# Kernel optimization log

Hardware: AMD Instinct MI355X
Metric: run time of the kernel (lower is better)

Reference implementation:

```python
import jax, jax.numpy as jnp
import numpy as np
from jax import lax

BS = 256
EPS = 1e-5  # torch LayerNorm default


def _layernorm(x, g, b):
    m = jnp.mean(x, axis=-1, keepdims=True)
    v = jnp.var(x, axis=-1, keepdims=True)
    return (x - m) / jnp.sqrt(v + EPS) * g + b


def _conv(x, w, b):
    y = lax.conv_general_dilated(x, w, (1, 1), 'VALID',
                                 dimension_numbers=('NCHW', 'OIHW', 'NCHW'))
    return y + b[None, :, None, None]


def _maxpool2(x):
    return lax.reduce_window(x, -jnp.inf, lax.max, (1, 1, 2, 2), (1, 1, 2, 2), 'VALID')


def setup_inputs() -> dict:
    key = jax.random.key(0)
    ks = iter(jax.random.split(key, 64))
    def rn(shape, scale=0.05):
        return jax.random.normal(next(ks), shape, dtype=jnp.float32) * scale
    return dict(
        t=jax.random.uniform(next(ks), (BS, 128, 128), dtype=jnp.float32) * 255.0,
        conv1_w=rn((32, 1, 3, 3)), conv1_b=rn((32,)),
        conv2_w=rn((32, 32, 3, 3)), conv2_b=rn((32,)),
        exp_w=rn((36, 64)), exp_b=rn((64,)),
        # 16 tile-attention modules x 4 heads x (64 -> 16)
        mh_wq=rn((16, 4, 64, 16)), mh_bq=rn((16, 4, 16)),
        mh_wk=rn((16, 4, 64, 16)), mh_bk=rn((16, 4, 16)),
        mh_wv=rn((16, 4, 64, 16)), mh_bv=rn((16, 4, 16)),
        mh_wo=rn((16, 64, 64)), mh_bo=rn((16, 64)),
        ln1_g=jnp.ones((64,), jnp.float32), ln1_b=jnp.zeros((64,), jnp.float32),
        # 2 XL layers x 8 heads x (2048 -> 256)
        xl_wq=rn((2, 8, 2048, 256)), xl_bq=rn((2, 8, 256)),
        xl_wk=rn((2, 8, 2048, 256)), xl_bk=rn((2, 8, 256)),
        xl_wv=rn((2, 8, 2048, 256)), xl_bv=rn((2, 8, 256)),
        xl_wo=rn((2, 2048, 2048)), xl_bo=rn((2, 2048)),
        xln_g=jnp.ones((2, 2048), jnp.float32), xln_b=jnp.zeros((2, 2048), jnp.float32),
        fl1_w=rn((32768, 512)), fl1_b=rn((512,)),
        fl2_w=rn((512, 128)), fl2_b=rn((128,)),
        fl3_w=rn((128, 25)), fl3_b=rn((25,)),
    )


def reference(t, conv1_w, conv1_b, conv2_w, conv2_b, exp_w, exp_b,
              mh_wq, mh_bq, mh_wk, mh_bk, mh_wv, mh_bv, mh_wo, mh_bo,
              ln1_g, ln1_b,
              xl_wq, xl_bq, xl_wk, xl_bk, xl_wv, xl_bv, xl_wo, xl_bo,
              xln_g, xln_b, fl1_w, fl1_b, fl2_w, fl2_b, fl3_w, fl3_b):
    # Eval-mode forward with discard_mem=True (fresh KV memory): every
    # AttentionHead attends over the current step only; dropout = identity.
    bs = t.shape[0]
    x = t / 255.0
    # 4x4 tiling of 32x32 patches -> (bs*16, 1, 32, 32)
    sliced = x.reshape(bs, 4, 32, 4, 32).transpose(0, 1, 3, 2, 4)
    x = sliced.reshape(bs * 16, 1, 32, 32)
    u = _maxpool2(_conv(x, conv1_w, conv1_b))        # (bs*16, 32, 15, 15)
    u = _maxpool2(_conv(u, conv2_w, conv2_b))        # (bs*16, 32, 6, 6)
    u = u.reshape(bs * 16, 32, 36)
    u = jax.nn.relu(u @ exp_w + exp_b)               # (bs*16, 32, 64)
    u = u.reshape(16, bs, 32, 64)                    # raw reshape, as in source

    # 16 multihead modules, 4 heads each, d_feature=16, seq_len=32
    q = jnp.einsum('mbsd,mhdf->mbhsf', u, mh_wq) + mh_bq[:, None, :, None, :]
    k = jnp.einsum('mbsd,mhdf->mbhsf', u, mh_wk) + mh_bk[:, None, :, None, :]
    v = jnp.einsum('mbsd,mhdf->mbhsf', u, mh_wv) + mh_bv[:, None, :, None, :]
    a = jax.nn.softmax(jnp.einsum('mbhsf,mbhtf->mbhst', q, k) / jnp.sqrt(16.0), axis=-1)
    o = jnp.einsum('mbhst,mbhtf->mbhsf', a, v)
    o = o.transpose(0, 1, 3, 2, 4).reshape(16, bs, 32, 64)  # concat heads
    o = jnp.einsum('mbsd,mde->mbse', o, mh_wo) + mh_bo[:, None, None, :]
    u = _layernorm(u + o, ln1_g, ln1_b)
    u = u.reshape(16, bs, 2048).transpose(1, 0, 2)   # (bs, 16, 2048)

    # XL stage (as written in source: att output is computed but discarded,
    # u = u + dropout(u) -> 2u under identity dropout, then LayerNorm)
    for i in range(2):
        q = jnp.einsum('bsd,hdf->bhsf', u, xl_wq[i]) + xl_bq[i][None, :, None, :]
        k = jnp.einsum('bsd,hdf->bhsf', u, xl_wk[i]) + xl_bk[i][None, :, None, :]
        vv = jnp.einsum('bsd,hdf->bhsf', u, xl_wv[i]) + xl_bv[i][None, :, None, :]
        aw = jax.nn.softmax(jnp.einsum('bhsf,bhtf->bhst', q, k) / jnp.sqrt(256.0), axis=-1)
        oo = jnp.einsum('bhst,bhtf->bhsf', aw, vv).transpose(0, 2, 1, 3).reshape(bs, 16, 2048)
        oo = oo @ xl_wo[i] + xl_bo[i]  # discarded, matching the source
        u = u + u
        u = _layernorm(u, xln_g[i], xln_b[i])

    u = u.reshape(bs, 16 * 2048)
    u = jax.nn.relu(u @ fl1_w + fl1_b)
    u = jax.nn.relu(u @ fl2_w + fl2_b)
    return u @ fl3_w + fl3_b
```

## Files before the change

### kernel.cpp

```cpp
#include <hip/hip_runtime.h>
#include <hip/hip_bf16.h>
#include <math.h>

#define LN_EPS 1e-5f

typedef __attribute__((ext_vector_type(8))) short short8v;
typedef __attribute__((ext_vector_type(4))) float f32x4;

static __device__ __forceinline__ unsigned short f2bf(float x) {
    unsigned u = __float_as_uint(x);
    u += 0x7fffu + ((u >> 16) & 1u);
    return (unsigned short)(u >> 16);
}
static __device__ __forceinline__ float bf2f(unsigned short h) {
    return __uint_as_float(((unsigned)h) << 16);
}

#define MFMA3(ACC, AH, AL, BH, BL)                                          \
    ACC = __builtin_amdgcn_mfma_f32_16x16x32_bf16(AH, BH, ACC, 0, 0, 0);    \
    ACC = __builtin_amdgcn_mfma_f32_16x16x32_bf16(AL, BH, ACC, 0, 0, 0);    \
    ACC = __builtin_amdgcn_mfma_f32_16x16x32_bf16(AH, BL, ACC, 0, 0, 0);

__global__ __launch_bounds__(512, 4) void k_conv(
    const float* __restrict__ t,
    const float* __restrict__ c1w, const float* __restrict__ c1b,
    const float* __restrict__ c2w, const float* __restrict__ c2b,
    const float* __restrict__ ew,  const float* __restrict__ eb,
    float* __restrict__ u)
{
    __shared__ __align__(16) unsigned short s_W2[2][9216];
    __shared__ __align__(16) unsigned short s_p1h[4 * 225 * 8];
    __shared__ __align__(16) unsigned short s_p1l[4 * 225 * 8];
    __shared__ __align__(16) float s_s2[32 * 36];
    __shared__ float s_c2b[32];

    float* s_x  = (float*)s_W2;
    float* s_ew = (float*)s_p1h;
    unsigned short* s_wh = s_W2[0];
    unsigned short* s_wl = s_W2[1];

    const int p   = blockIdx.x;
    const int tid = threadIdx.x;

    const int b = p >> 4, tile = p & 15, tr = tile >> 2, tc = tile & 3;
    const float* tp = t + (size_t)b * 128 * 128 + (size_t)tr * 32 * 128 + tc * 32;
    for (int i = tid; i < 1024; i += 512) {
        const int r = i >> 5, c = i & 31;
        s_x[r * 33 + c] = tp[r * 128 + c] * (1.0f / 255.0f);
    }
    if (tid < 32) s_c2b[tid] = c2b[tid];
    __syncthreads();

    if ((tid & 255) < 225) {
        const int pos  = tid & 255;
        const int half = tid >> 8;
        const int pi = pos / 15, pj = pos % 15;
        float xw[16];
        #pragma unroll
        for (int r = 0; r < 4; ++r)
            #pragma unroll
            for (int c = 0; c < 4; ++c)
                xw[r * 4 + c] = s_x[(2 * pi + r) * 33 + (2 * pj + c)];
        #pragma unroll
        for (int og2 = 0; og2 < 2; ++og2) {
            const int og = half * 2 + og2;
            short8v hb, lb;
            #pragma unroll
            for (int o = 0; o < 8; ++o) {
                const int oc = og * 8 + o;
                float w[9];
                #pragma unroll
                for (int j = 0; j < 9; ++j) w[j] = c1w[oc * 9 + j];
                float mx = -3.0e38f;
                #pragma unroll
                for (int a = 0; a < 2; ++a)
                    #pragma unroll
                    for (int bb = 0; bb < 2; ++bb) {
                        float s = xw[(a + 0) * 4 + bb + 0] * w[0]
                                + xw[(a + 0) * 4 + bb + 1] * w[1]
                                + xw[(a + 0) * 4 + bb + 2] * w[2]
                                + xw[(a + 1) * 4 + bb + 0] * w[3]
                                + xw[(a + 1) * 4 + bb + 1] * w[4]
                                + xw[(a + 1) * 4 + bb + 2] * w[5]
                                + xw[(a + 2) * 4 + bb + 0] * w[6]
                                + xw[(a + 2) * 4 + bb + 1] * w[7]
                                + xw[(a + 2) * 4 + bb + 2] * w[8];
                        mx = fmaxf(mx, s);
                    }
                const float val = mx + c1b[oc];
                const unsigned short h = f2bf(val);
                hb[o] = (short)h;
                lb[o] = (short)f2bf(val - bf2f(h));
// ... 66 lines not shown
            for (int mt = 0; mt < 2; ++mt)
                #pragma unroll
                for (int r = 0; r < 4; ++r) {
                    float v = (mt == 0) ? acc0[r] : acc1[r];
                    v = fmaxf(v, __shfl_xor(v, 1));
                    v = fmaxf(v, __shfl_xor(v, 2));
                    if ((lane & 3) == 0) {
                        const int oc = mt * 16 + (lane >> 4) * 4 + r;
                        const int pq2 = nt * 4 + (jcol >> 2);
                        s_s2[oc * 36 + pq2] = v + s_c2b[oc];
                    }
                }
        }

        if (w8 < 2) {
            const int nt = 8;
            const int mt = w8;
            const int n = nt * 16 + jcol;
            const int pq = n >> 2, w4 = n & 3;
            const int pi = pq / 6, pj = pq - pi * 6;
            const int rbase = 2 * pi + (w4 >> 1);
            const int cbase = 2 * pj + (w4 & 1);

            f32x4 accX = {0,0,0,0};
            #pragma unroll
            for (int ks = 0; ks < 9; ++ks) {
                const int dr = ks / 3, dc = ks - dr * 3;
                const int ab = ks * 1024 + lg * 256 + jcol * 8 + mt * 128;
                const short8v ah = *(const short8v*)&s_wh[ab];
                const short8v al = *(const short8v*)&s_wl[ab];
                const int wpos = (rbase + dr) * 15 + (cbase + dc);
                const int boff = lg * 1800 + wpos * 8;
                const short8v bh = *(const short8v*)&s_p1h[boff];
                const short8v bl = *(const short8v*)&s_p1l[boff];
                accX = __builtin_amdgcn_mfma_f32_16x16x32_bf16(ah, bh, accX, 0, 0, 0);
                accX = __builtin_amdgcn_mfma_f32_16x16x32_bf16(al, bh, accX, 0, 0, 0);
                accX = __builtin_amdgcn_mfma_f32_16x16x32_bf16(ah, bl, accX, 0, 0, 0);
            }
            #pragma unroll
            for (int r = 0; r < 4; ++r) {
                float v = accX[r];
                v = fmaxf(v, __shfl_xor(v, 1));
                v = fmaxf(v, __shfl_xor(v, 2));
                if ((lane & 3) == 0) {
                    const int oc = mt * 16 + (lane >> 4) * 4 + r;
                    const int pq2 = nt * 4 + (jcol >> 2);
                    s_s2[oc * 36 + pq2] = v + s_c2b[oc];
                }
            }
        }
    }
    __syncthreads();

    for (int i = tid; i < 576; i += 512)
        *(float4*)&s_ew[i * 4] = *(const float4*)&ew[i * 4];
    __syncthreads();

    {
        const int s  = tid >> 4;
        const int e0 = (tid & 15) * 4;
        float acc4[4];
        *(float4*)&acc4[0] = *(const float4*)&eb[e0];
        for (int f = 0; f < 36; ++f) {
            const float sv = s_s2[s * 36 + f];
            const float4 w0 = *(const float4*)&s_ew[f * 64 + e0];
            acc4[0] += sv * w0.x; acc4[1] += sv * w0.y;
            acc4[2] += sv * w0.z; acc4[3] += sv * w0.w;
        }
        float4 o0;
        o0.x = fmaxf(acc4[0], 0.0f); o0.y = fmaxf(acc4[1], 0.0f);
        o0.z = fmaxf(acc4[2], 0.0f); o0.w = fmaxf(acc4[3], 0.0f);
        *(float4*)&u[(size_t)p * 2048 + s * 64 + e0] = o0;
    }
}

__global__ __launch_bounds__(256, 2) void k_attn(
    const float* __restrict__ u,
    const float* __restrict__ wq, const float* __restrict__ bq,
    const float* __restrict__ wk, const float* __restrict__ bk,
    const float* __restrict__ wv, const float* __restrict__ bv,
    const float* __restrict__ wo, const float* __restrict__ bo,
    const float* __restrict__ g1, const float* __restrict__ b1,
    const float* __restrict__ xg, const float* __restrict__ xb,
    unsigned short* __restrict__ Ah, unsigned short* __restrict__ Al)
{
    __shared__ __align__(16) unsigned short s_w[2][64 * 64];
    __shared__ __align__(16) float s_uf[32 * 68];
    __shared__ __align__(16) unsigned short R1[12288];
    __shared__ __align__(16) unsigned short R2[5632];
    __shared__ float s_red[2][32][2];
    __shared__ float s_red2[2][4][2];

    unsigned short* qA_h = R1;
    unsigned short* qA_l = R1 + 3072;
    unsigned short* kB_h = R1 + 6144;
    unsigned short* kB_l = R1 + 9216;
    unsigned short* p_h  = R1;
    unsigned short* p_l  = R1 + 5120;
    unsigned short* vT_h = R2;
    unsigned short* vT_l = R2 + 2560;
    unsigned short* oA_h = R2;
    unsigned short* oA_l = R2 + 2816;

    const int g   = blockIdx.x;
    const int m   = g >> 8;
    const int b2  = g & 255;
    const int tid = threadIdx.x;
    const int l   = tid & 63;
    const int w   = tid >> 6;
    const int l15 = l & 15;
    const int lg  = l >> 4;

    {
        const int s = tid >> 3, dq = (tid & 7) * 8;
        const float* up = u + (size_t)g * 2048 + s * 64 + dq;
        *(float4*)&s_uf[s * 68 + dq]     = *(const float4*)up;
        *(float4*)&s_uf[s * 68 + dq + 4] = *(const float4*)(up + 4);
    }

    const int wn  = tid & 63;
    const int wkq = tid >> 6;
    float wreg[16];

    #define LOADQKV(SRC)                                                          \
        {                                                                         \
            const float* sp = (SRC) + (size_t)m * 4096 + (wn >> 4) * 1024 + (wn & 15); \
            _Pragma("unroll")                                                     \
            for (int j = 0; j < 16; ++j) wreg[j] = sp[(wkq * 16 + j) * 16];       \
        }
    #define LOADO(SRC)                                                            \
        {                                                                         \
            const float* sp = (SRC) + (size_t)m * 4096 + wn;                      \
            _Pragma("unroll")                                                     \
            for (int j = 0; j < 16; ++j) wreg[j] = sp[(wkq * 16 + j) * 64];       \
        }
    #define WRITEW()                                                              \
        {                                                                         \
            _Pragma("unroll")                                                     \
            for (int j2 = 0; j2 < 8; ++j2) {                                      \
                const int d = wkq * 16 + j2 * 2;                                  \
                const float v0 = wreg[j2 * 2], v1 = wreg[j2 * 2 + 1];             \
                const unsigned short h0 = f2bf(v0), h1 = f2bf(v1);                \
                const unsigned short q0 = f2bf(v0 - bf2f(h0));                    \
                const unsigned short q1 = f2bf(v1 - bf2f(h1));                    \
                const int idx = wn * 64 + (((d >> 3) ^ (wn & 7)) << 3) + (d & 7); \
                *(unsigned*)&s_w[0][idx] = (unsigned)h0 | ((unsigned)h1 << 16);   \
                *(unsigned*)&s_w[1][idx] = (unsigned)q0 | ((unsigned)q1 << 16);   \
            }                                                                     \
        }

    LOADQKV(wq);
    __syncthreads();
    WRITEW();

    short8v uh[2][2], ul[2][2];
    #pragma unroll
    for (int mf = 0; mf < 2; ++mf)
        #pragma unroll
        for (int ks = 0; ks < 2; ++ks) {
            const float* pb = &s_uf[(mf * 16 + l15) * 68 + (ks * 4 + lg) * 8];
            float xv[8];
            *(float4*)&xv[0] = *(const float4*)pb;
            *(float4*)&xv[4] = *(const float4*)(pb + 4);
            short8v hh, ll;
            #pragma unroll
            for (int j = 0; j < 8; ++j) {
                const unsigned short h = f2bf(xv[j]);
                hh[j] = (short)h;
                ll[j] = (short)f2bf(xv[j] - bf2f(h));
            }
            uh[mf][ks] = hh; ul[mf][ks] = ll;
        }
    __syncthreads();

    #define PROJ(BIAS, MODE)                                                      \
        {                                                                         \
            short8v wbh[2], wbl[2];                                               \
            const int bn = w * 16 + l15;                                          \
            _Pragma("unroll")                                                     \
            for (int ks = 0; ks < 2; ++ks) {                                      \
                const int off = bn * 64 + (((ks * 4 + lg) ^ (bn & 7)) << 3);      \
                wbh[ks] = *(const short8v*)&s_w[0][off];                          \
                wbl[ks] = *(const short8v*)&s_w[1][off];                          \
            }                                                                     \
            const float bias_v = (BIAS)[m * 64 + bn];                             \
            f32x4 a0 = {0,0,0,0}, a1 = {0,0,0,0};                                 \
            _Pragma("unroll")                                                     \
            for (int ks = 0; ks < 2; ++ks) {                                      \
                MFMA3(a0, uh[0][ks], ul[0][ks], wbh[ks], wbl[ks]);                \
                MFMA3(a1, uh[1][ks], ul[1][ks], wbh[ks], wbl[ks]);                \
            }                                                                     \
            _Pragma("unroll")                                                     \
            for (int mf = 0; mf < 2; ++mf) {                                      \
                const f32x4 av = mf ? a1 : a0;                                    \
                _Pragma("unroll")                                                 \
                for (int r = 0; r < 4; ++r) {                                     \
                    const float val = av[r] + bias_v;                             \
                    const unsigned short hh = f2bf(val);                          \
                    const unsigned short lo = f2bf(val - bf2f(hh));               \
                    const int srow = mf * 16 + lg * 4 + r;                        \
                    if ((MODE) == 0) { const int ix = w * 768 + srow * 24 + l15;  \
                        qA_h[ix] = hh; qA_l[ix] = lo; }                           \
                    else if ((MODE) == 1) { const int ix = w * 768 + srow * 24 + l15; \
                        kB_h[ix] = hh; kB_l[ix] = lo; }                           \
                    else { const int ix = w * 640 + l15 * 40 + srow;              \
                        vT_h[ix] = hh; vT_l[ix] = lo; }                           \
                }                                                                 \
            }                                                                     \
        }

    PROJ(bq, 0);
    LOADQKV(wk);
    __syncthreads();
    WRITEW();
    __syncthreads();

    PROJ(bk, 1);
    LOADQKV(wv);
    __syncthreads();
    WRITEW();
    __syncthreads();

    PROJ(bv, 2);
    LOADO(wo);
    __syncthreads();
    WRITEW();
    __syncthreads();

    float pvreg[2][2][4];
    {
        const short8v zz = {0,0,0,0,0,0,0,0};
        short8v qh[2], ql[2], kh[2], kl[2];
        const bool kreal = (lg < 2);
        #pragma unroll
        for (int mf = 0; mf < 2; ++mf) {
            if (kreal) {
                const int ia = w * 768 + (mf * 16 + l15) * 24 + lg * 8;
                qh[mf] = *(const short8v*)&qA_h[ia];
                ql[mf] = *(const short8v*)&qA_l[ia];
                kh[mf] = *(const short8v*)&kB_h[ia];
                kl[mf] = *(const short8v*)&kB_l[ia];
            } else { qh[mf] = zz; ql[mf] = zz; kh[mf] = zz; kl[mf] = zz; }
        }
        f32x4 sc[2][2];
        #pragma unroll
        for (int mf = 0; mf < 2; ++mf)
            #pragma unroll
            for (int nf = 0; nf < 2; ++nf) {
                sc[mf][nf] = (f32x4){0,0,0,0};
                MFMA3(sc[mf][nf], qh[mf], ql[mf], kh[nf], kl[nf]);
            }
        #pragma unroll
        for (int mf = 0; mf < 2; ++mf)
            #pragma unroll
            for (int r = 0; r < 4; ++r) {
                const float v0 = sc[mf][0][r] * 0.25f;
                const float v1 = sc[mf][1][r] * 0.25f;
                float mx = fmaxf(v0, v1);
                mx = fmaxf(mx, __shfl_xor(mx, 1));
                mx = fmaxf(mx, __shfl_xor(mx, 2));
                mx = fmaxf(mx, __shfl_xor(mx, 4));
                mx = fmaxf(mx, __shfl_xor(mx, 8));
                const float e0 = expf(v0 - mx), e1 = expf(v1 - mx);
                float sm = e0 + e1;
                sm += __shfl_xor(sm, 1);
                sm += __shfl_xor(sm, 2);
                sm += __shfl_xor(sm, 4);
                sm += __shfl_xor(sm, 8);
                const float inv = 1.0f / sm;
                pvreg[mf][0][r] = e0 * inv;
                pvreg[mf][1][r] = e1 * inv;
            }
    }
    __syncthreads();

    #pragma unroll
    for (int mf = 0; mf < 2; ++mf)
        #pragma unroll
        for (int nf = 0; nf < 2; ++nf)
            #pragma unroll
            for (int r = 0; r < 4; ++r) {
                const int srow = mf * 16 + lg * 4 + r;
                const int tt = nf * 16 + l15;
                const int ix = w * 1280 + srow * 40 + tt;
                const float val = pvreg[mf][nf][r];
                const unsigned short hh = f2bf(val);
                p_h[ix] = hh;
                p_l[ix] = f2bf(val - bf2f(hh));
            }
    __syncthreads();

    f32x4 ov[2];
    {
        short8v ph[2], pl[2], vh_, vl_;
        #pragma unroll
        for (int mf = 0; mf < 2; ++mf) {
            const int ix = w * 1280 + (mf * 16 + l15) * 40 + lg * 8;
            ph[mf] = *(const short8v*)&p_h[ix];
            pl[mf] = *(const short8v*)&p_l[ix];
        }
        const int iv = w * 640 + l15 * 40 + lg * 8;
        vh_ = *(const short8v*)&vT_h[iv];
        vl_ = *(const short8v*)&vT_l[iv];
        #pragma unroll
        for (int mf = 0; mf < 2; ++mf) {
            ov[mf] = (f32x4){0,0,0,0};
            MFMA3(ov[mf], ph[mf], pl[mf], vh_, vl_);
        }
    }
    __syncthreads();

    #pragma unroll
    for (int mf = 0; mf < 2; ++mf)
        #pragma unroll
        for (int r = 0; r < 4; ++r) {
            const int srow = mf * 16 + lg * 4 + r;
            const int dd = w * 16 + l15;
            const int ix = srow * 88 + dd;
            const float val = ov[mf][r];
            const unsigned short hh = f2bf(val);
            oA_h[ix] = hh;
            oA_l[ix] = f2bf(val - bf2f(hh));
        }
    __syncthreads();

    const int mfA = w >> 1;
    const int nfb = (w & 1) * 2;
    float x[2][4];
    {
        short8v oh[2], ol[2];
        #pragma unroll
        for (int ks = 0; ks < 2; ++ks) {
            const int ix = (mfA * 16 + l15) * 88 + (ks * 4 + lg) * 8;
            oh[ks] = *(const short8v*)&oA_h[ix];
            ol[ks] = *(const short8v*)&oA_l[ix];
        }
        #pragma unroll
        for (int nfi = 0; nfi < 2; ++nfi) {
            const int n = (nfb + nfi) * 16 + l15;
            f32x4 xe = {0,0,0,0};
            #pragma unroll
            for (int ks = 0; ks < 2; ++ks) {
                const int off = n * 64 + (((ks * 4 + lg) ^ (n & 7)) << 3);
                const short8v wbh = *(const short8v*)&s_w[0][off];
                const short8v wbl = *(const short8v*)&s_w[1][off];
                MFMA3(xe, oh[ks], ol[ks], wbh, wbl);
            }
            const int e = n;
            const float bo_v = bo[m * 64 + e];
            #pragma unroll
            for (int r = 0; r < 4; ++r) {
                const int srow = mfA * 16 + lg * 4 + r;
                x[nfi][r] = xe[r] + bo_v + s_uf[srow * 68 + e];
            }
        }
    }
    #pragma unroll
    for (int r = 0; r < 4; ++r) {
        float s1 = x[0][r] + x[1][r];
        float s2 = x[0][r] * x[0][r] + x[1][r] * x[1][r];
        s1 += __shfl_xor(s1, 1); s2 += __shfl_xor(s2, 1);
        s1 += __shfl_xor(s1, 2); s2 += __shfl_xor(s2, 2);
        s1 += __shfl_xor(s1, 4); s2 += __shfl_xor(s2, 4);
        s1 += __shfl_xor(s1, 8); s2 += __shfl_xor(s2, 8);
        if (l15 == 0) {
            const int srow = mfA * 16 + lg * 4 + r;
            s_red[w & 1][srow][0] = s1;
            s_red[w & 1][srow][1] = s2;
        }
    }
    __syncthreads();

    float q2[2][4];
    #pragma unroll
    for (int r = 0; r < 4; ++r) {
        const int srow = mfA * 16 + lg * 4 + r;
        const float sum = s_red[0][srow][0] + s_red[1][srow][0];
        const float ssq = s_red[0][srow][1] + s_red[1][srow][1];
        const float mean = sum * (1.0f / 64.0f);
        const float var = fmaxf(ssq * (1.0f / 64.0f) - mean * mean, 0.0f);
        const float inv = rsqrtf(var + LN_EPS);
        #pragma unroll
        for (int nfi = 0; nfi < 2; ++nfi) {
            const int e = (nfb + nfi) * 16 + l15;
            const float y = (x[nfi][r] - mean) * inv * g1[e] + b1[e];
            q2[nfi][r] = 2.0f * y;
        }
    }

    #pragma unroll
    for (int L = 0; L < 2; ++L) {
        float ls = 0.0f, lq = 0.0f;
        #pragma unroll
        for (int nfi = 0; nfi < 2; ++nfi)
            #pragma unroll
            for (int r = 0; r < 4; ++r) { ls += q2[nfi][r]; lq += q2[nfi][r] * q2[nfi][r]; }
        ls += __shfl_xor(ls, 1);  lq += __shfl_xor(lq, 1);
        ls += __shfl_xor(ls, 2);  lq += __shfl_xor(lq, 2);
        ls += __shfl_xor(ls, 4);  lq += __shfl_xor(lq, 4);
        ls += __shfl_xor(ls, 8);  lq += __shfl_xor(lq, 8);
        ls += __shfl_xor(ls, 16); lq += __shfl_xor(lq, 16);
        ls += __shfl_xor(ls, 32); lq += __shfl_xor(lq, 32);
        if (l == 0) { s_red2[L][w][0] = ls; s_red2[L][w][1] = lq; }
        __syncthreads();
        const float sum = s_red2[L][0][0] + s_red2[L][1][0] + s_red2[L][2][0] + s_red2[L][3][0];
        const float ssq = s_red2[L][0][1] + s_red2[L][1][1] + s_red2[L][2][1] + s_red2[L][3][1];
        const float mean = sum * (1.0f / 2048.0f);
        const float var = fmaxf(ssq * (1.0f / 2048.0f) - mean * mean, 0.0f);
        const float inv = rsqrtf(var + LN_EPS);
        #pragma unroll
        for (int nfi = 0; nfi < 2; ++nfi)
            #pragma unroll
            for (int r = 0; r < 4; ++r) {
                const int srow = mfA * 16 + lg * 4 + r;
                const int e = (nfb + nfi) * 16 + l15;
                const int col = srow * 64 + e;
                const float z = (q2[nfi][r] - mean) * inv * xg[L * 2048 + col] + xb[L * 2048 + col];
                q2[nfi][r] = (L == 0) ? 2.0f * z : z;
            }
    }

    #pragma unroll
    for (int nfi = 0; nfi < 2; ++nfi)
        #pragma unroll
        for (int r = 0; r < 4; ++r) {
            const int srow = mfA * 16 + lg * 4 + r;
            const int e = (nfb + nfi) * 16 + l15;
            const int col = srow * 64 + e;
            const float val = q2[nfi][r];
            const unsigned short hh = f2bf(val);
            const size_t addr = ((size_t)(m * 64 + (col >> 5)) * 256 + b2) * 32 + (col & 31);
            Ah[addr] = hh;
            Al[addr] = f2bf(val - bf2f(hh));
        }
}

__global__ __launch_bounds__(512) void k_fl1(
    const unsigned short* __restrict__ Ah,
    const unsigned short* __restrict__ Al,
    const float* __restrict__ W,
    float* __restrict__ part)
{
    __shared__ __align__(16) unsigned short s_wh[128 * 64];
    __shared__ __align__(16) unsigned short s_wl[128 * 64];

    const int nb  = blockIdx.x;
    const int kb  = blockIdx.y;
    const int tid = threadIdx.x;
    const int lane = tid & 63;
    const int wid  = tid >> 6;
    const int wm = wid >> 1;
    const int wn = wid & 1;

    const int sn = tid & 127;
    const int sq = tid >> 7;
    const int k0 = kb * 512;

    f32x4 acc[4][4];
    #pragma unroll
    for (int i = 0; i < 4; ++i)
        #pragma unroll
        for (int j = 0; j < 4; ++j)
            acc[i][j] = (f32x4){0.0f, 0.0f, 0.0f, 0.0f};

    float wreg[16];
    {
        const float* wp = W + (size_t)(k0 + sq * 16) * 512 + nb * 128 + sn;
        #pragma unroll
        for (int j = 0; j < 16; ++j) wreg[j] = wp[(size_t)j * 512];
    }

    const int hsn = sn & 7;
    const int wbase = sn * 64;
    const int wo0 = (((sq * 2) ^ hsn) << 3);
    const int wo1 = (((sq * 2 + 1) ^ hsn) << 3);

    for (int tt = 0; tt < 8; ++tt) {
        __syncthreads();
        {
            short8v h0, h1, l0, l1;
            #pragma unroll
            for (int j = 0; j < 8; ++j) {
                const unsigned short ha = f2bf(wreg[j]);
                const unsigned short hb = f2bf(wreg[j + 8]);
                h0[j] = (short)ha;
                h1[j] = (short)hb;
                l0[j] = (short)f2bf(wreg[j] - bf2f(ha));
// ... 81 lines not shown

    if (tid < 128) {
        float acc = fb2[tid];
        for (int k = 0; k < 512; k++) acc += s_u1[k] * w2[k * 128 + tid];
        s_u2[tid] = fmaxf(acc, 0.0f);
    }
    __syncthreads();

    if (tid < 25) {
        float acc = fb3[tid];
        for (int k = 0; k < 128; k++) acc += s_u2[k] * w3[k * 25 + tid];
        out[r * 25 + tid] = acc;
    }
}

extern "C" void kernel_launch(void* const* d_in, const int* in_sizes, int n_in,
                              void* d_out, int out_size, void* d_ws, size_t ws_size,
                              hipStream_t stream)
{
    const float* t      = (const float*)d_in[0];
    const float* c1w    = (const float*)d_in[1];
    const float* c1b    = (const float*)d_in[2];
    const float* c2w    = (const float*)d_in[3];
    const float* c2b    = (const float*)d_in[4];
    const float* ew     = (const float*)d_in[5];
    const float* eb     = (const float*)d_in[6];
    const float* mh_wq  = (const float*)d_in[7];
    const float* mh_bq  = (const float*)d_in[8];
    const float* mh_wk  = (const float*)d_in[9];
    const float* mh_bk  = (const float*)d_in[10];
    const float* mh_wv  = (const float*)d_in[11];
    const float* mh_bv  = (const float*)d_in[12];
    const float* mh_wo  = (const float*)d_in[13];
    const float* mh_bo  = (const float*)d_in[14];
    const float* ln1_g  = (const float*)d_in[15];
    const float* ln1_b  = (const float*)d_in[16];
    const float* xln_g  = (const float*)d_in[25];
    const float* xln_b  = (const float*)d_in[26];
    const float* fl1_w  = (const float*)d_in[27];
    const float* fl1_b  = (const float*)d_in[28];
    const float* fl2_w  = (const float*)d_in[29];
    const float* fl2_b  = (const float*)d_in[30];
    const float* fl3_w  = (const float*)d_in[31];
    const float* fl3_b  = (const float*)d_in[32];
    (void)in_sizes; (void)n_in; (void)out_size; (void)ws_size;

    float* U   = (float*)d_ws;
    float* U2  = U + 8388608;
    unsigned short* Ah = (unsigned short*)U2;
    unsigned short* Al = Ah + 8388608;
    float* PART = U;
    float* out  = (float*)d_out;

    k_conv<<<4096, 512, 0, stream>>>(t, c1w, c1b, c2w, c2b, ew, eb, U);
    k_attn<<<4096, 256, 0, stream>>>(U, mh_wq, mh_bq, mh_wk, mh_bk, mh_wv, mh_bv,
                                     mh_wo, mh_bo, ln1_g, ln1_b, xln_g, xln_b,
                                     Ah, Al);
    k_fl1<<<dim3(4, 64), 512, 0, stream>>>(Ah, Al, fl1_w, PART);
    k_tail<<<256, 256, 0, stream>>>(PART, fl1_b, fl2_w, fl2_b, fl3_w, fl3_b, out);
}
```

Measured before the change: 271.9 us.

## Process two batch items per attention block to share staged weights

Each k_attn block now runs 512 threads covering two batch samples of the same tile module. The bf16 hi/lo weight conversion into shared memory is split across all 512 threads and shared by both halves, halving per-sample weight load and conversion work and the block count. Per-sample scratch buffers and reduction arrays are duplicated per half, which raises shared memory per block and may reduce occupancy. Block-wide syncs now also couple the two halves.

```diff
diff --git a/kernel.cpp b/kernel.cpp
--- a/kernel.cpp
+++ b/kernel.cpp
@@ -232,7 +232,7 @@
     }
 }
 
-__global__ __launch_bounds__(256, 2) void k_attn(
+__global__ __launch_bounds__(512, 2) void k_attn(
     const float* __restrict__ u,
     const float* __restrict__ wq, const float* __restrict__ bq,
     const float* __restrict__ wk, const float* __restrict__ bk,
@@ -243,60 +243,63 @@
     unsigned short* __restrict__ Ah, unsigned short* __restrict__ Al)
 {
     __shared__ __align__(16) unsigned short s_w[2][64 * 64];
-    __shared__ __align__(16) float s_uf[32 * 68];
-    __shared__ __align__(16) unsigned short R1[12288];
-    __shared__ __align__(16) unsigned short R2[5632];
-    __shared__ float s_red[2][32][2];
-    __shared__ float s_red2[2][4][2];
-
-    unsigned short* qA_h = R1;
-    unsigned short* qA_l = R1 + 3072;
-    unsigned short* kB_h = R1 + 6144;
-    unsigned short* kB_l = R1 + 9216;
-    unsigned short* p_h  = R1;
-    unsigned short* p_l  = R1 + 5120;
-    unsigned short* vT_h = R2;
-    unsigned short* vT_l = R2 + 2560;
-    unsigned short* oA_h = R2;
-    unsigned short* oA_l = R2 + 2816;
+    __shared__ __align__(16) float s_uf2[2][32 * 68];
+    __shared__ __align__(16) unsigned short R1[2][12288];
+    __shared__ __align__(16) unsigned short R2[2][5632];
+    __shared__ float s_red[2][2][32][2];
+    __shared__ float s_red2[2][2][4][2];
 
     const int g   = blockIdx.x;
-    const int m   = g >> 8;
-    const int b2  = g & 255;
+    const int m   = g >> 7;
     const int tid = threadIdx.x;
-    const int l   = tid & 63;
-    const int w   = tid >> 6;
+    const int bh  = tid >> 8;
+    const int t2  = tid & 255;
+    const int b2  = (g & 127) * 2 + bh;
+    const int l   = t2 & 63;
+    const int w   = t2 >> 6;
     const int l15 = l & 15;
     const int lg  = l >> 4;
 
+    float* s_uf = s_uf2[bh];
+    unsigned short* qA_h = R1[bh];
+    unsigned short* qA_l = R1[bh] + 3072;
+    unsigned short* kB_h = R1[bh] + 6144;
+    unsigned short* kB_l = R1[bh] + 9216;
+    unsigned short* p_h  = R1[bh];
+    unsigned short* p_l  = R1[bh] + 5120;
+    unsigned short* vT_h = R2[bh];
+    unsigned short* vT_l = R2[bh] + 2560;
+    unsigned short* oA_h = R2[bh];
+    unsigned short* oA_l = R2[bh] + 2816;
+
     {
-        const int s = tid >> 3, dq = (tid & 7) * 8;
-        const float* up = u + (size_t)g * 2048 + s * 64 + dq;
+        const int s = t2 >> 3, dq = (t2 & 7) * 8;
+        const float* up = u + (size_t)(m * 256 + b2) * 2048 + s * 64 + dq;
         *(float4*)&s_uf[s * 68 + dq]     = *(const float4*)up;
         *(float4*)&s_uf[s * 68 + dq + 4] = *(const float4*)(up + 4);
     }
 
-    const int wn  = tid & 63;
-    const int wkq = tid >> 6;
-    float wreg[16];
+    const int wn   = tid & 63;
+    const int wkq8 = tid >> 6;
+    float wreg[8];
 
     #define LOADQKV(SRC)                                                          \
         {                                                                         \
             const float* sp = (SRC) + (size_t)m * 4096 + (wn >> 4) * 1024 + (wn & 15); \
             _Pragma("unroll")                                                     \
-            for (int j = 0; j < 16; ++j) wreg[j] = sp[(wkq * 16 + j) * 16];       \
+            for (int j = 0; j < 8; ++j) wreg[j] = sp[(wkq8 * 8 + j) * 16];        \
         }
     #define LOADO(SRC)                                                            \
         {                                                                         \
             const float* sp = (SRC) + (size_t)m * 4096 + wn;                      \
             _Pragma("unroll")                                                     \
-            for (int j = 0; j < 16; ++j) wreg[j] = sp[(wkq * 16 + j) * 64];       \
+            for (int j = 0; j < 8; ++j) wreg[j] = sp[(wkq8 * 8 + j) * 64];        \
         }
     #define WRITEW()                                                              \
         {                                                                         \
             _Pragma("unroll")                                                     \
-            for (int j2 = 0; j2 < 8; ++j2) {                                      \
-                const int d = wkq * 16 + j2 * 2;                                  \
+            for (int j2 = 0; j2 < 4; ++j2) {                                      \
+                const int d = wkq8 * 8 + j2 * 2;                                  \
                 const float v0 = wreg[j2 * 2], v1 = wreg[j2 * 2 + 1];             \
                 const unsigned short h0 = f2bf(v0), h1 = f2bf(v1);                \
                 const unsigned short q0 = f2bf(v0 - bf2f(h0));                    \
@@ -523,8 +526,8 @@
         s1 += __shfl_xor(s1, 8); s2 += __shfl_xor(s2, 8);
         if (l15 == 0) {
             const int srow = mfA * 16 + lg * 4 + r;
-            s_red[w & 1][srow][0] = s1;
-            s_red[w & 1][srow][1] = s2;
+            s_red[bh][w & 1][srow][0] = s1;
+            s_red[bh][w & 1][srow][1] = s2;
         }
     }
     __syncthreads();
@@ -533,8 +536,8 @@
     #pragma unroll
     for (int r = 0; r < 4; ++r) {
         const int srow = mfA * 16 + lg * 4 + r;
-        const float sum = s_red[0][srow][0] + s_red[1][srow][0];
-        const float ssq = s_red[0][srow][1] + s_red[1][srow][1];
+        const float sum = s_red[bh][0][srow][0] + s_red[bh][1][srow][0];
+        const float ssq = s_red[bh][0][srow][1] + s_red[bh][1][srow][1];
         const float mean = sum * (1.0f / 64.0f);
         const float var = fmaxf(ssq * (1.0f / 64.0f) - mean * mean, 0.0f);
         const float inv = rsqrtf(var + LN_EPS);
@@ -559,10 +562,12 @@
         ls += __shfl_xor(ls, 8);  lq += __shfl_xor(lq, 8);
         ls += __shfl_xor(ls, 16); lq += __shfl_xor(lq, 16);
         ls += __shfl_xor(ls, 32); lq += __shfl_xor(lq, 32);
-        if (l == 0) { s_red2[L][w][0] = ls; s_red2[L][w][1] = lq; }
+        if (l == 0) { s_red2[bh][L][w][0] = ls; s_red2[bh][L][w][1] = lq; }
         __syncthreads();
-        const float sum = s_red2[L][0][0] + s_red2[L][1][0] + s_red2[L][2][0] + s_red2[L][3][0];
-        const float ssq = s_red2[L][0][1] + s_red2[L][1][1] + s_red2[L][2][1] + s_red2[L][3][1];
+        const float sum = s_red2[bh][L][0][0] + s_red2[bh][L][1][0]
+                        + s_red2[bh][L][2][0] + s_red2[bh][L][3][0];
+        const float ssq = s_red2[bh][L][0][1] + s_red2[bh][L][1][1]
+                        + s_red2[bh][L][2][1] + s_red2[bh][L][3][1];
         const float mean = sum * (1.0f / 2048.0f);
         const float var = fmaxf(ssq * (1.0f / 2048.0f) - mean * mean, 0.0f);
         const float inv = rsqrtf(var + LN_EPS);
@@ -779,7 +784,7 @@
     float* out  = (float*)d_out;
 
     k_conv<<<4096, 512, 0, stream>>>(t, c1w, c1b, c2w, c2b, ew, eb, U);
-    k_attn<<<4096, 256, 0, stream>>>(U, mh_wq, mh_bq, mh_wk, mh_bk, mh_wv, mh_bv,
+    k_attn<<<2048, 512, 0, stream>>>(U, mh_wq, mh_bq, mh_wk, mh_bk, mh_wv, mh_bv,
                                      mh_wo, mh_bo, ln1_g, ln1_b, xln_g, xln_b,
                                      Ah, Al);
     k_fl1<<<dim3(4, 64), 512, 0, stream>>>(Ah, Al, fl1_w, PART);
```

Result: no change. 275.0 us (+1.1%).

## Fuse conv/expand kernel with tile-attention kernel to keep activations in LDS

Applied to the files above, without the earlier changes.

Merges the convolution/expansion kernel and the tile-attention plus LayerNorm kernel into one kernel. The expanded activations go into shared memory instead of a global round trip, and the shared buffers are aliased so both stages fit in one block's LDS. The first Q weight load is issued early so it overlaps the expansion step. The attention stages run on only half of the 512 threads, and the larger fused LDS footprint may lower occupancy.

```diff
diff --git a/kernel.cpp b/kernel.cpp
--- a/kernel.cpp
+++ b/kernel.cpp
@@ -21,23 +21,46 @@
     ACC = __builtin_amdgcn_mfma_f32_16x16x32_bf16(AL, BH, ACC, 0, 0, 0);    \
     ACC = __builtin_amdgcn_mfma_f32_16x16x32_bf16(AH, BL, ACC, 0, 0, 0);
 
-__global__ __launch_bounds__(512, 4) void k_conv(
+__global__ __launch_bounds__(512, 4) void k_fused(
     const float* __restrict__ t,
     const float* __restrict__ c1w, const float* __restrict__ c1b,
     const float* __restrict__ c2w, const float* __restrict__ c2b,
     const float* __restrict__ ew,  const float* __restrict__ eb,
-    float* __restrict__ u)
+    const float* __restrict__ wq, const float* __restrict__ bq,
+    const float* __restrict__ wk, const float* __restrict__ bk,
+    const float* __restrict__ wv, const float* __restrict__ bv,
+    const float* __restrict__ wo, const float* __restrict__ bo,
+    const float* __restrict__ g1, const float* __restrict__ b1,
+    const float* __restrict__ xg, const float* __restrict__ xb,
+    unsigned short* __restrict__ Ah, unsigned short* __restrict__ Al)
 {
     __shared__ __align__(16) unsigned short s_W2[2][9216];
-    __shared__ __align__(16) unsigned short s_p1h[4 * 225 * 8];
-    __shared__ __align__(16) unsigned short s_p1l[4 * 225 * 8];
-    __shared__ __align__(16) float s_s2[32 * 36];
+    __shared__ __align__(16) unsigned short s_p1[14400];
+    __shared__ __align__(16) float s_s2[1152];
+    __shared__ __align__(16) float s_uf[32 * 68];
     __shared__ float s_c2b[32];
 
     float* s_x  = (float*)s_W2;
-    float* s_ew = (float*)s_p1h;
-    unsigned short* s_wh = s_W2[0];
-    unsigned short* s_wl = s_W2[1];
+    unsigned short* s_wh  = s_W2[0];
+    unsigned short* s_wl  = s_W2[1];
+    unsigned short* s_p1h = s_p1;
+    unsigned short* s_p1l = s_p1 + 7200;
+    float* s_ew = (float*)s_p1;
+    unsigned short* aw_h = s_W2[0];
+    unsigned short* aw_l = s_W2[0] + 4096;
+    unsigned short* R1   = s_p1;
+    unsigned short* R2   = s_W2[1];
+    unsigned short* qA_h = R1;
+    unsigned short* qA_l = R1 + 3072;
+    unsigned short* kB_h = R1 + 6144;
+    unsigned short* kB_l = R1 + 9216;
+    unsigned short* p_h  = R1;
+    unsigned short* p_l  = R1 + 5120;
+    unsigned short* vT_h = R2;
+    unsigned short* vT_l = R2 + 2560;
+    unsigned short* oA_h = R2;
+    unsigned short* oA_l = R2 + 2816;
+    float* s_redf = s_s2;
 
     const int p   = blockIdx.x;
     const int tid = threadIdx.x;
@@ -210,8 +233,42 @@
     }
     __syncthreads();
 
+    const int m2 = p >> 8;
+    const int b2 = p & 255;
+    const int wn   = tid & 63;
+    const int wkq8 = tid >> 6;
+    float wreg[8];
+
+    #define LOADQKV(SRC)                                                          \
+        {                                                                         \
+            const float* sp = (SRC) + (size_t)m2 * 4096 + (wn >> 4) * 1024 + (wn & 15); \
+            _Pragma("unroll")                                                     \
+            for (int j = 0; j < 8; ++j) wreg[j] = sp[(wkq8 * 8 + j) * 16];        \
+        }
+    #define LOADO(SRC)                                                            \
+        {                                                                         \
+            const float* sp = (SRC) + (size_t)m2 * 4096 + wn;                     \
+            _Pragma("unroll")                                                     \
+            for (int j = 0; j < 8; ++j) wreg[j] = sp[(wkq8 * 8 + j) * 64];        \
+        }
+    #define WRITEW()                                                              \
+        {                                                                         \
+            _Pragma("unroll")                                                     \
+            for (int j2 = 0; j2 < 4; ++j2) {                                      \
+                const int d = wkq8 * 8 + j2 * 2;                                  \
+                const float v0 = wreg[j2 * 2], v1 = wreg[j2 * 2 + 1];             \
+                const unsigned short h0 = f2bf(v0), h1 = f2bf(v1);                \
+                const unsigned short q0 = f2bf(v0 - bf2f(h0));                    \
+                const unsigned short q1 = f2bf(v1 - bf2f(h1));                    \
+                const int idx = wn * 64 + (((d >> 3) ^ (wn & 7)) << 3) + (d & 7); \
+                *(unsigned*)&aw_h[idx] = (unsigned)h0 | ((unsigned)h1 << 16);     \
+                *(unsigned*)&aw_l[idx] = (unsigned)q0 | ((unsigned)q1 << 16);     \
+            }                                                                     \
+        }
+
     for (int i = tid; i < 576; i += 512)
         *(float4*)&s_ew[i * 4] = *(const float4*)&ew[i * 4];
+    LOADQKV(wq);
     __syncthreads();
 
     {
@@ -228,120 +285,50 @@
         float4 o0;
         o0.x = fmaxf(acc4[0], 0.0f); o0.y = fmaxf(acc4[1], 0.0f);
         o0.z = fmaxf(acc4[2], 0.0f); o0.w = fmaxf(acc4[3], 0.0f);
-        *(float4*)&u[(size_t)p * 2048 + s * 64 + e0] = o0;
-    }
-}
-
-__global__ __launch_bounds__(256, 2) void k_attn(
-    const float* __restrict__ u,
-    const float* __restrict__ wq, const float* __restrict__ bq,
-    const float* __restrict__ wk, const float* __restrict__ bk,
-    const float* __restrict__ wv, const float* __restrict__ bv,
-    const float* __restrict__ wo, const float* __restrict__ bo,
-    const float* __restrict__ g1, const float* __restrict__ b1,
-    const float* __restrict__ xg, const float* __restrict__ xb,
-    unsigned short* __restrict__ Ah, unsigned short* __restrict__ Al)
-{
-    __shared__ __align__(16) unsigned short s_w[2][64 * 64];
-    __shared__ __align__(16) float s_uf[32 * 68];
-    __shared__ __align__(16) unsigned short R1[12288];
-    __shared__ __align__(16) unsigned short R2[5632];
-    __shared__ float s_red[2][32][2];
-    __shared__ float s_red2[2][4][2];
-
-    unsigned short* qA_h = R1;
-    unsigned short* qA_l = R1 + 3072;
-    unsigned short* kB_h = R1 + 6144;
-    unsigned short* kB_l = R1 + 9216;
-    unsigned short* p_h  = R1;
-    unsigned short* p_l  = R1 + 5120;
-    unsigned short* vT_h = R2;
-    unsigned short* vT_l = R2 + 2560;
-    unsigned short* oA_h = R2;
-    unsigned short* oA_l = R2 + 2816;
-
-    const int g   = blockIdx.x;
-    const int m   = g >> 8;
-    const int b2  = g & 255;
-    const int tid = threadIdx.x;
+        *(float4*)&s_uf[s * 68 + e0] = o0;
+    }
+    __syncthreads();
+
     const int l   = tid & 63;
     const int w   = tid >> 6;
     const int l15 = l & 15;
     const int lg  = l >> 4;
 
-    {
-        const int s = tid >> 3, dq = (tid & 7) * 8;
-        const float* up = u + (size_t)g * 2048 + s * 64 + dq;
-        *(float4*)&s_uf[s * 68 + dq]     = *(const float4*)up;
-        *(float4*)&s_uf[s * 68 + dq + 4] = *(const float4*)(up + 4);
-    }
-
-    const int wn  = tid & 63;
-    const int wkq = tid >> 6;
-    float wreg[16];
-
-    #define LOADQKV(SRC)                                                          \
-        {                                                                         \
-            const float* sp = (SRC) + (size_t)m * 4096 + (wn >> 4) * 1024 + (wn & 15); \
-            _Pragma("unroll")                                                     \
-            for (int j = 0; j < 16; ++j) wreg[j] = sp[(wkq * 16 + j) * 16];       \
-        }
-    #define LOADO(SRC)                                                            \
-        {                                                                         \
-            const float* sp = (SRC) + (size_t)m * 4096 + wn;                      \
-            _Pragma("unroll")                                                     \
-            for (int j = 0; j < 16; ++j) wreg[j] = sp[(wkq * 16 + j) * 64];       \
-        }
-    #define WRITEW()                                                              \
-        {                                                                         \
-            _Pragma("unroll")                                                     \
-            for (int j2 = 0; j2 < 8; ++j2) {                                      \
-                const int d = wkq * 16 + j2 * 2;                                  \
-                const float v0 = wreg[j2 * 2], v1 = wreg[j2 * 2 + 1];             \
-                const unsigned short h0 = f2bf(v0), h1 = f2bf(v1);                \
-                const unsigned short q0 = f2bf(v0 - bf2f(h0));                    \
-                const unsigned short q1 = f2bf(v1 - bf2f(h1));                    \
-                const int idx = wn * 64 + (((d >> 3) ^ (wn & 7)) << 3) + (d & 7); \
-                *(unsigned*)&s_w[0][idx] = (unsigned)h0 | ((unsigned)h1 << 16);   \
-                *(unsigned*)&s_w[1][idx] = (unsigned)q0 | ((unsigned)q1 << 16);   \
-            }                                                                     \
-        }
-
-    LOADQKV(wq);
-    __syncthreads();
     WRITEW();
 
     short8v uh[2][2], ul[2][2];
-    #pragma unroll
-    for (int mf = 0; mf < 2; ++mf)
-        #pragma unroll
-        for (int ks = 0; ks < 2; ++ks) {
-            const float* pb = &s_uf[(mf * 16 + l15) * 68 + (ks * 4 + lg) * 8];
-            float xv[8];
-            *(float4*)&xv[0] = *(const float4*)pb;
-            *(float4*)&xv[4] = *(const float4*)(pb + 4);
-            short8v hh, ll;
-            #pragma unroll
-            for (int j = 0; j < 8; ++j) {
-                const unsigned short h = f2bf(xv[j]);
-                hh[j] = (short)h;
-                ll[j] = (short)f2bf(xv[j] - bf2f(h));
-            }
-            uh[mf][ks] = hh; ul[mf][ks] = ll;
-        }
+    if (tid < 256) {
+        #pragma unroll
+        for (int mf = 0; mf < 2; ++mf)
+            #pragma unroll
+            for (int ks = 0; ks < 2; ++ks) {
+                const float* pb = &s_uf[(mf * 16 + l15) * 68 + (ks * 4 + lg) * 8];
+                float xv[8];
+                *(float4*)&xv[0] = *(const float4*)pb;
+                *(float4*)&xv[4] = *(const float4*)(pb + 4);
+                short8v hh, ll;
+                #pragma unroll
+                for (int j = 0; j < 8; ++j) {
+                    const unsigned short h = f2bf(xv[j]);
+                    hh[j] = (short)h;
+                    ll[j] = (short)f2bf(xv[j] - bf2f(h));
+                }
+                uh[mf][ks] = hh; ul[mf][ks] = ll;
+            }
+    }
     __syncthreads();
 
     #define PROJ(BIAS, MODE)                                                      \
-        {                                                                         \
+        if (tid < 256) {                                                          \
             short8v wbh[2], wbl[2];                                               \
             const int bn = w * 16 + l15;                                          \
             _Pragma("unroll")                                                     \
             for (int ks = 0; ks < 2; ++ks) {                                      \
                 const int off = bn * 64 + (((ks * 4 + lg) ^ (bn & 7)) << 3);      \
-                wbh[ks] = *(const short8v*)&s_w[0][off];                          \
-                wbl[ks] = *(const short8v*)&s_w[1][off];                          \
+                wbh[ks] = *(const short8v*)&aw_h[off];                            \
+                wbl[ks] = *(const short8v*)&aw_l[off];                            \
             }                                                                     \
-            const float bias_v = (BIAS)[m * 64 + bn];                             \
+            const float bias_v = (BIAS)[m2 * 64 + bn];                            \
             f32x4 a0 = {0,0,0,0}, a1 = {0,0,0,0};                                 \
             _Pragma("unroll")                                                     \
             for (int ks = 0; ks < 2; ++ks) {                                      \
@@ -386,7 +373,7 @@
     __syncthreads();
 
     float pvreg[2][2][4];
-    {
+    if (tid < 256) {
         const short8v zz = {0,0,0,0,0,0,0,0};
         short8v qh[2], ql[2], kh[2], kl[2];
         const bool kreal = (lg < 2);
@@ -432,24 +419,26 @@
     }
     __syncthreads();
 
-    #pragma unroll
-    for (int mf = 0; mf < 2; ++mf)
-        #pragma unroll
-        for (int nf = 0; nf < 2; ++nf)
-            #pragma unroll
-            for (int r = 0; r < 4; ++r) {
-                const int srow = mf * 16 + lg * 4 + r;
-                const int tt = nf * 16 + l15;
-                const int ix = w * 1280 + srow * 40 + tt;
-                const float val = pvreg[mf][nf][r];
-                const unsigned short hh = f2bf(val);
-                p_h[ix] = hh;
-                p_l[ix] = f2bf(val - bf2f(hh));
-            }
+    if (tid < 256) {
+        #pragma unroll
+        for (int mf = 0; mf < 2; ++mf)
+            #pragma unroll
+            for (int nf = 0; nf < 2; ++nf)
+                #pragma unroll
+                for (int r = 0; r < 4; ++r) {
+                    const int srow = mf * 16 + lg * 4 + r;
+                    const int tt = nf * 16 + l15;
+                    const int ix = w * 1280 + srow * 40 + tt;
+                    const float val = pvreg[mf][nf][r];
+                    const unsigned short hh = f2bf(val);
+                    p_h[ix] = hh;
+                    p_l[ix] = f2bf(val - bf2f(hh));
+                }
+    }
     __syncthreads();
 
     f32x4 ov[2];
-    {
+    if (tid < 256) {
         short8v ph[2], pl[2], vh_, vl_;
         #pragma unroll
         for (int mf = 0; mf < 2; ++mf) {
@@ -468,24 +457,26 @@
     }
     __syncthreads();
 
-    #pragma unroll
-    for (int mf = 0; mf < 2; ++mf)
-        #pragma unroll
-        for (int r = 0; r < 4; ++r) {
-            const int srow = mf * 16 + lg * 4 + r;
-            const int dd = w * 16 + l15;
-            const int ix = srow * 88 + dd;
-            const float val = ov[mf][r];
-            const unsigned short hh = f2bf(val);
-            oA_h[ix] = hh;
-            oA_l[ix] = f2bf(val - bf2f(hh));
-        }
-    __syncthreads();
-
-    const int mfA = w >> 1;
+    if (tid < 256) {
+        #pragma unroll
+        for (int mf = 0; mf < 2; ++mf)
+            #pragma unroll
+            for (int r = 0; r < 4; ++r) {
+                const int srow = mf * 16 + lg * 4 + r;
+                const int dd = w * 16 + l15;
+                const int ix = srow * 88 + dd;
+                const float val = ov[mf][r];
+                const unsigned short hh = f2bf(val);
+                oA_h[ix] = hh;
+                oA_l[ix] = f2bf(val - bf2f(hh));
+            }
+    }
+    __syncthreads();
+
+    const int mfA = (w & 3) >> 1;
     const int nfb = (w & 1) * 2;
     float x[2][4];
-    {
+    if (tid < 256) {
         short8v oh[2], ol[2];
         #pragma unroll
         for (int ks = 0; ks < 2; ++ks) {
@@ -500,72 +491,95 @@
             #pragma unroll
             for (int ks = 0; ks < 2; ++ks) {
                 const int off = n * 64 + (((ks * 4 + lg) ^ (n & 7)) << 3);
-                const short8v wbh = *(const short8v*)&s_w[0][off];
-                const short8v wbl = *(const short8v*)&s_w[1][off];
+                const short8v wbh = *(const short8v*)&aw_h[off];
+                const short8v wbl = *(const short8v*)&aw_l[off];
                 MFMA3(xe, oh[ks], ol[ks], wbh, wbl);
             }
-            const int e = n;
-            const float bo_v = bo[m * 64 + e];
+            const float bo_v = bo[m2 * 64 + n];
             #pragma unroll
             for (int r = 0; r < 4; ++r) {
                 const int srow = mfA * 16 + lg * 4 + r;
-                x[nfi][r] = xe[r] + bo_v + s_uf[srow * 68 + e];
-            }
-        }
-    }
-    #pragma unroll
-    for (int r = 0; r < 4; ++r) {
-        float s1 = x[0][r] + x[1][r];
-        float s2 = x[0][r] * x[0][r] + x[1][r] * x[1][r];
-        s1 += __shfl_xor(s1, 1); s2 += __shfl_xor(s2, 1);
-        s1 += __shfl_xor(s1, 2); s2 += __shfl_xor(s2, 2);
-        s1 += __shfl_xor(s1, 4); s2 += __shfl_xor(s2, 4);
-        s1 += __shfl_xor(s1, 8); s2 += __shfl_xor(s2, 8);
-        if (l15 == 0) {
+                x[nfi][r] = xe[r] + bo_v + s_uf[srow * 68 + n];
+            }
+        }
+        #pragma unroll
+        for (int r = 0; r < 4; ++r) {
+            float s1 = x[0][r] + x[1][r];
+            float s2 = x[0][r] * x[0][r] + x[1][r] * x[1][r];
+            s1 += __shfl_xor(s1, 1); s2 += __shfl_xor(s2, 1);
+            s1 += __shfl_xor(s1, 2); s2 += __shfl_xor(s2, 2);
+            s1 += __shfl_xor(s1, 4); s2 += __shfl_xor(s2, 4);
+            s1 += __shfl_xor(s1, 8); s2 += __shfl_xor(s2, 8);
+            if (l15 == 0) {
+                const int srow = mfA * 16 + lg * 4 + r;
+                s_redf[(w & 1) * 64 + srow * 2 + 0] = s1;
+                s_redf[(w & 1) * 64 + srow * 2 + 1] = s2;
+            }
+        }
+    }
+    __syncthreads();
+
+    float q2[2][4];
+    if (tid < 256) {
+        #pragma unroll
+        for (int r = 0; r < 4; ++r) {
             const int srow = mfA * 16 + lg * 4 + r;
-            s_red[w & 1][srow][0] = s1;
-            s_red[w & 1][srow][1] = s2;
-        }
-    }
-    __syncthreads();
-
-    float q2[2][4];
-    #pragma unroll
-    for (int r = 0; r < 4; ++r) {
-        const int srow = mfA * 16 + lg * 4 + r;
-        const float sum = s_red[0][srow][0] + s_red[1][srow][0];
-        const float ssq = s_red[0][srow][1] + s_red[1][srow][1];
-        const float mean = sum * (1.0f / 64.0f);
-        const float var = fmaxf(ssq * (1.0f / 64.0f) - mean * mean, 0.0f);
-        const float inv = rsqrtf(var + LN_EPS);
-        #pragma unroll
-        for (int nfi = 0; nfi < 2; ++nfi) {
-            const int e = (nfb + nfi) * 16 + l15;
-            const float y = (x[nfi][r] - mean) * inv * g1[e] + b1[e];
-            q2[nfi][r] = 2.0f * y;
+            const float sum = s_redf[srow * 2 + 0] + s_redf[64 + srow * 2 + 0];
+            const float ssq = s_redf[srow * 2 + 1] + s_redf[64 + srow * 2 + 1];
+            const float mean = sum * (1.0f / 64.0f);
+            const float var = fmaxf(ssq * (1.0f / 64.0f) - mean * mean, 0.0f);
+            const float inv = rsqrtf(var + LN_EPS);
+            #pragma unroll
+            for (int nfi = 0; nfi < 2; ++nfi) {
+                const int e = (nfb + nfi) * 16 + l15;
+                const float y = (x[nfi][r] - mean) * inv * g1[e] + b1[e];
+                q2[nfi][r] = 2.0f * y;
+            }
         }
     }
 
     #pragma unroll
     for (int L = 0; L < 2; ++L) {
-        float ls = 0.0f, lq = 0.0f;
-        #pragma unroll
-        for (int nfi = 0; nfi < 2; ++nfi)
-            #pragma unroll
-            for (int r = 0; r < 4; ++r) { ls += q2[nfi][r]; lq += q2[nfi][r] * q2[nfi][r]; }
-        ls += __shfl_xor(ls, 1);  lq += __shfl_xor(lq, 1);
-        ls += __shfl_xor(ls, 2);  lq += __shfl_xor(lq, 2);
-        ls += __shfl_xor(ls, 4);  lq += __shfl_xor(lq, 4);
-        ls += __shfl_xor(ls, 8);  lq += __shfl_xor(lq, 8);
-        ls += __shfl_xor(ls, 16); lq += __shfl_xor(lq, 16);
-        ls += __shfl_xor(ls, 32); lq += __shfl_xor(lq, 32);
-        if (l == 0) { s_red2[L][w][0] = ls; s_red2[L][w][1] = lq; }
+        if (tid < 256) {
+            float ls = 0.0f, lq = 0.0f;
+            #pragma unroll
+            for (int nfi = 0; nfi < 2; ++nfi)
+                #pragma unroll
+                for (int r = 0; r < 4; ++r) { ls += q2[nfi][r]; lq += q2[nfi][r] * q2[nfi][r]; }
+            ls += __shfl_xor(ls, 1);  lq += __shfl_xor(lq, 1);
+            ls += __shfl_xor(ls, 2);  lq += __shfl_xor(lq, 2);
+            ls += __shfl_xor(ls, 4);  lq += __shfl_xor(lq, 4);
+            ls += __shfl_xor(ls, 8);  lq += __shfl_xor(lq, 8);
+            ls += __shfl_xor(ls, 16); lq += __shfl_xor(lq, 16);
+            ls += __shfl_xor(ls, 32); lq += __shfl_xor(lq, 32);
+            if (l == 0) {
+                s_redf[128 + L * 8 + w * 2 + 0] = ls;
+                s_redf[128 + L * 8 + w * 2 + 1] = lq;
+            }
+        }
         __syncthreads();
-        const float sum = s_red2[L][0][0] + s_red2[L][1][0] + s_red2[L][2][0] + s_red2[L][3][0];
-        const float ssq = s_red2[L][0][1] + s_red2[L][1][1] + s_red2[L][2][1] + s_red2[L][3][1];
-        const float mean = sum * (1.0f / 2048.0f);
-        const float var = fmaxf(ssq * (1.0f / 2048.0f) - mean * mean, 0.0f);
-        const float inv = rsqrtf(var + LN_EPS);
+        if (tid < 256) {
+            const float sum = s_redf[128 + L * 8 + 0] + s_redf[128 + L * 8 + 2]
+                            + s_redf[128 + L * 8 + 4] + s_redf[128 + L * 8 + 6];
+            const float ssq = s_redf[128 + L * 8 + 1] + s_redf[128 + L * 8 + 3]
+                            + s_redf[128 + L * 8 + 5] + s_redf[128 + L * 8 + 7];
+            const float mean = sum * (1.0f / 2048.0f);
+            const float var = fmaxf(ssq * (1.0f / 2048.0f) - mean * mean, 0.0f);
+            const float inv = rsqrtf(var + LN_EPS);
+            #pragma unroll
+            for (int nfi = 0; nfi < 2; ++nfi)
+                #pragma unroll
+                for (int r = 0; r < 4; ++r) {
+                    const int srow = mfA * 16 + lg * 4 + r;
+                    const int e = (nfb + nfi) * 16 + l15;
+                    const int col = srow * 64 + e;
+                    const float z = (q2[nfi][r] - mean) * inv * xg[L * 2048 + col] + xb[L * 2048 + col];
+                    q2[nfi][r] = (L == 0) ? 2.0f * z : z;
+                }
+        }
+    }
+
+    if (tid < 256) {
         #pragma unroll
         for (int nfi = 0; nfi < 2; ++nfi)
             #pragma unroll
@@ -573,24 +587,17 @@
                 const int srow = mfA * 16 + lg * 4 + r;
                 const int e = (nfb + nfi) * 16 + l15;
                 const int col = srow * 64 + e;
-                const float z = (q2[nfi][r] - mean) * inv * xg[L * 2048 + col] + xb[L * 2048 + col];
-                q2[nfi][r] = (L == 0) ? 2.0f * z : z;
-            }
-    }
-
-    #pragma unroll
-    for (int nfi = 0; nfi < 2; ++nfi)
-        #pragma unroll
-        for (int r = 0; r < 4; ++r) {
-            const int srow = mfA * 16 + lg * 4 + r;
-            const int e = (nfb + nfi) * 16 + l15;
-            const int col = srow * 64 + e;
-            const float val = q2[nfi][r];
-            const unsigned short hh = f2bf(val);
-            const size_t addr = ((size_t)(m * 64 + (col >> 5)) * 256 + b2) * 32 + (col & 31);
-            Ah[addr] = hh;
-            Al[addr] = f2bf(val - bf2f(hh));
-        }
+                const float val = q2[nfi][r];
+                const unsigned short hh = f2bf(val);
+                const size_t addr = ((size_t)(m2 * 64 + (col >> 5)) * 256 + b2) * 32 + (col & 31);
+                Ah[addr] = hh;
+                Al[addr] = f2bf(val - bf2f(hh));
+            }
+    }
+    #undef LOADQKV
+    #undef LOADO
+    #undef WRITEW
+    #undef PROJ
 }
 
 __global__ __launch_bounds__(512) void k_fl1(
@@ -778,10 +785,10 @@
     float* PART = U;
     float* out  = (float*)d_out;
 
-    k_conv<<<4096, 512, 0, stream>>>(t, c1w, c1b, c2w, c2b, ew, eb, U);
-    k_attn<<<4096, 256, 0, stream>>>(U, mh_wq, mh_bq, mh_wk, mh_bk, mh_wv, mh_bv,
-                                     mh_wo, mh_bo, ln1_g, ln1_b, xln_g, xln_b,
-                                     Ah, Al);
+    k_fused<<<4096, 512, 0, stream>>>(t, c1w, c1b, c2w, c2b, ew, eb,
+                                      mh_wq, mh_bq, mh_wk, mh_bk, mh_wv, mh_bv,
+                                      mh_wo, mh_bo, ln1_g, ln1_b, xln_g, xln_b,
+                                      Ah, Al);
     k_fl1<<<dim3(4, 64), 512, 0, stream>>>(Ah, Al, fl1_w, PART);
     k_tail<<<256, 256, 0, stream>>>(PART, fl1_b, fl2_w, fl2_b, fl3_w, fl3_b, out);
 }
```

Result: faster. 266.3 us (-2.1%).
